# Performance work log

Measured on AMD Instinct MI355X. Metric: run time of the kernel, lower is better.

Reference implementation:

```python
import jax, jax.numpy as jnp
import numpy as np

B, T = 64, 20
VOCAB, E, CE, ANS = 20000, 300, 1024, 3000
H, N, W, R = 512, 256, 64, 4
RW = R * W
IF_SIZES = [RW, R, W, 1, W, W, R, 1, 1, 3 * R]  # read_keys, read_str, write_key, write_str, erase, write_vec, free, alloc_g, write_g, modes
IF_TOT = sum(IF_SIZES)
CLIP = 20.0
EPS = 1e-6


def _cosine_weights(mem, keys, strengths):
    # mem [B,N,W], keys [B,K,W], strengths [B,K] -> softmax over N
    mem_n = mem / (jnp.linalg.norm(mem, axis=-1, keepdims=True) + EPS)
    key_n = keys / (jnp.linalg.norm(keys, axis=-1, keepdims=True) + EPS)
    sim = jnp.einsum('bkw,bnw->bkn', key_n, mem_n)
    return jax.nn.softmax(sim * strengths[..., None], axis=-1)


def _init_state(b):
    z = lambda *s: jnp.zeros(s, jnp.float32)
    return (z(b, N, W), z(b, N, N), z(b, N), z(b, R, N), z(b, N), z(b, N), z(b, R, W), z(b, H), z(b, H))


def _dnc_step(Wih, Whh, b, Wif, bif, Wout, bout, state, x):
    mem, link, prec, wr, ww, usage, rvec, h, c = state
    bsz = x.shape[0]
    inp = jnp.concatenate([x, rvec.reshape(bsz, RW)], -1)
    gates = inp @ Wih + h @ Whh + b
    gi, gf, gg, go = jnp.split(gates, 4, -1)
    c = jax.nn.sigmoid(gf) * c + jax.nn.sigmoid(gi) * jnp.tanh(gg)
    h = jax.nn.sigmoid(go) * jnp.tanh(c)
    hc = jnp.clip(h, -CLIP, CLIP)
    xi = hc @ Wif + bif
    p = jnp.split(xi, np.cumsum(IF_SIZES)[:-1].tolist(), axis=-1)
    read_keys = jnp.tanh(p[0]).reshape(bsz, R, W)
    read_str = jax.nn.softplus(p[1])
    write_key = jnp.tanh(p[2]).reshape(bsz, 1, W)
    write_str = jax.nn.softplus(p[3])
    erase = jax.nn.sigmoid(p[4])
    write_vec = jnp.tanh(p[5])
    free = jax.nn.sigmoid(p[6])
    alloc_g = jax.nn.sigmoid(p[7])
    write_g = jax.nn.sigmoid(p[8])
    modes = jax.nn.softmax(p[9].reshape(bsz, R, 3), -1)

    # usage update and allocation (sort-based, data dependent)
    psi = jnp.prod(1.0 - free[..., None] * wr, axis=1)          # [B,N]
    usage = (usage + ww - usage * ww) * psi
    s_idx = jnp.argsort(usage, axis=-1)                          # ascending usage
    s_u = jnp.take_along_axis(usage, s_idx, -1)
    cp = jnp.cumprod(jnp.concatenate([jnp.ones_like(s_u[:, :1]), s_u[:, :-1]], -1), -1)
    a_sorted = (1.0 - s_u) * cp
    inv = jnp.argsort(s_idx, axis=-1)
    alloc = jnp.take_along_axis(a_sorted, inv, -1)

    # write
    cw = _cosine_weights(mem, write_key, write_str)[:, 0]        # [B,N]
    ww = write_g * (alloc_g * alloc + (1.0 - alloc_g) * cw)
    mem = mem * (1.0 - ww[..., None] * erase[:, None, :]) + ww[..., None] * write_vec[:, None, :]

    # temporal link matrix
    link = (1.0 - ww[:, :, None] - ww[:, None, :]) * link + ww[:, :, None] * prec[:, None, :]
    link = link * (1.0 - jnp.eye(N, dtype=link.dtype))
    prec = (1.0 - ww.sum(-1, keepdims=True)) * prec + ww

    # read
    fw = jnp.einsum('bij,brj->bri', link, wr)
    bw = jnp.einsum('bji,brj->bri', link, wr)
    cr = _cosine_weights(mem, read_keys, read_str)
    wr = modes[..., 0:1] * bw + modes[..., 1:2] * cr + modes[..., 2:3] * fw
    rvec = jnp.einsum('brn,bnw->brw', wr, mem)

    out = jnp.concatenate([hc, rvec.reshape(bsz, RW)], -1) @ Wout + bout
    out = jnp.clip(out, -CLIP, CLIP)
    return (mem, link, prec, wr, ww, usage, rvec, h, c), out


def _model(img_feat, emb, img_W, img_b, q_Wih, q_Whh, q_b, q_Wif, q_bif, q_Wout, q_bout,
           c_Wih, c_Whh, c_b, c_Wif, c_bif, c_Wout, c_bout, fc1_W, fc1_b, fc2_W, fc2_b, qst):
    bsz = qst.shape[0]
    # question encoder: embedding -> tanh -> DNC over time -> mean pool
    qv = jnp.tanh(emb[qst])                                      # [B,T,E]
    step = lambda st, x: _dnc_step(q_Wih, q_Whh, q_b, q_Wif, q_bif, q_Wout, q_bout, st, x)
    _, outs = jax.lax.scan(step, _init_state(bsz), jnp.swapaxes(qv, 0, 1))
    qfeat = outs.mean(0)                                         # [B,CE]
    # image encoder: fc on frozen VGG feature, L2 norm (norm detached)
    imgf = img_feat @ img_W + img_b
    imgf = imgf / jax.lax.stop_gradient(jnp.linalg.norm(imgf, axis=1, keepdims=True))
    comb = jnp.tanh(imgf * qfeat)
    # controller DNC: single timestep
    st_c, out_c = _dnc_step(c_Wih, c_Whh, c_b, c_Wif, c_bif, c_Wout, c_bout, _init_state(bsz), comb)
    rv_c = st_c[6].reshape(bsz, RW)
    last = jnp.tanh(jnp.concatenate([out_c, rv_c], -1))
    last = jnp.tanh(last @ fc1_W + fc1_b)
    return last @ fc2_W + fc2_b                                  # logits [B,ANS]


def setup_inputs():
    ks = jax.random.split(jax.random.key(0), 20)
    g = lambda k, s, sc=0.05: jax.random.normal(k, s, dtype=jnp.float32) * sc
    z = lambda *s: jnp.zeros(s, jnp.float32)
    return {
        'img_feat': g(ks[0], (B, 4096), 1.0),
        'qst': jax.random.randint(ks[1], (B, T), 0, VOCAB),
        'emb': g(ks[2], (VOCAB, E)),
        'img_W': g(ks[3], (4096, CE)), 'img_b': z(CE),
        'q_Wih': g(ks[4], (E + RW, 4 * H)), 'q_Whh': g(ks[5], (H, 4 * H)), 'q_b': z(4 * H),
        'q_Wif': g(ks[6], (H, IF_TOT)), 'q_bif': z(IF_TOT),
        'q_Wout': g(ks[7], (H + RW, CE)), 'q_bout': z(CE),
        'c_Wih': g(ks[8], (CE + RW, 4 * H)), 'c_Whh': g(ks[9], (H, 4 * H)), 'c_b': z(4 * H),
        'c_Wif': g(ks[10], (H, IF_TOT)), 'c_bif': z(IF_TOT),
        'c_Wout': g(ks[11], (H + RW, CE)), 'c_bout': z(CE),
        'fc1_W': g(ks[12], (CE + RW, ANS)), 'fc1_b': z(ANS),
        'fc2_W': g(ks[13], (ANS, ANS)), 'fc2_b': z(ANS),
    }


def reference(img_feat, qst, emb, img_W, img_b, q_Wih, q_Whh, q_b, q_Wif, q_bif, q_Wout, q_bout,
              c_Wih, c_Whh, c_b, c_Wif, c_bif, c_Wout, c_bout, fc1_W, fc1_b, fc2_W, fc2_b):
    return _model(img_feat, emb, img_W, img_b, q_Wih, q_Whh, q_b, q_Wif, q_bif, q_Wout, q_bout,
                  c_Wih, c_Whh, c_b, c_Wif, c_bif, c_Wout, c_bout, fc1_W, fc1_b, fc2_W, fc2_b, qst)
```

## Files before the change

kernel.cpp:

```cpp
#include <hip/hip_runtime.h>
#include <cmath>

#define CLIPV 20.0f
#define EPSV 1e-6f

__device__ __forceinline__ float sigmoidf_(float x){ return 1.0f/(1.0f + expf(-x)); }
__device__ __forceinline__ float softplusf_(float x){ return (x > 20.0f) ? x : log1pf(expf(x)); }
__device__ __forceinline__ float clipf_(float x){ return fminf(fmaxf(x, -CLIPV), CLIPV); }

__device__ __forceinline__ float wave_sum64(float v){
  #pragma unroll
  for (int off=32; off>=1; off>>=1) v += __shfl_xor(v, off, 64);
  return v;
}
__device__ __forceinline__ float wave_max64(float v){
  #pragma unroll
  for (int off=32; off>=1; off>>=1) v = fmaxf(v, __shfl_xor(v, off, 64));
  return v;
}
__device__ __forceinline__ float block_sum256(float v, float* s_red){
  v = wave_sum64(v);
  __syncthreads();
  if ((threadIdx.x & 63) == 0) s_red[threadIdx.x>>6] = v;
  __syncthreads();
  return s_red[0]+s_red[1]+s_red[2]+s_red[3];
}
__device__ __forceinline__ float block_max256(float v, float* s_red){
  v = wave_max64(v);
  __syncthreads();
  if ((threadIdx.x & 63) == 0) s_red[threadIdx.x>>6] = v;
  __syncthreads();
  return fmaxf(fmaxf(s_red[0],s_red[1]), fmaxf(s_red[2],s_red[3]));
}
template<int N>
__device__ __forceinline__ void block_sumN(float (&v)[N], float* scr){
  #pragma unroll
  for (int i=0;i<N;i++) v[i] = wave_sum64(v[i]);
  __syncthreads();
  if ((threadIdx.x & 63) == 0){
    int w = threadIdx.x >> 6;
    #pragma unroll
    for (int i=0;i<N;i++) scr[w*N + i] = v[i];
  }
  __syncthreads();
  #pragma unroll
  for (int i=0;i<N;i++) v[i] = scr[0*N+i] + scr[1*N+i] + scr[2*N+i] + scr[3*N+i];
}
template<int N>
__device__ __forceinline__ void block_maxN(float (&v)[N], float* scr){
  #pragma unroll
  for (int i=0;i<N;i++) v[i] = wave_max64(v[i]);
  __syncthreads();
  if ((threadIdx.x & 63) == 0){
    int w = threadIdx.x >> 6;
    #pragma unroll
    for (int i=0;i<N;i++) scr[w*N + i] = v[i];
  }
  __syncthreads();
  #pragma unroll
  for (int i=0;i<N;i++) v[i] = fmaxf(fmaxf(scr[0*N+i],scr[1*N+i]), fmaxf(scr[2*N+i],scr[3*N+i]));
}

__device__ __forceinline__ void cstore(float* p, float v){
  __hip_atomic_store(p, v, __ATOMIC_RELAXED, __HIP_MEMORY_SCOPE_AGENT);
}

#define WS_MEM    0
#define WS_LINK   1048576
#define WS_PREC   5242880
#define WS_WR     5275648
#define WS_WW     5341184
#define WS_USAGE  5357568
#define WS_BAR    5373952
#define WS_ZONEA  5374976
#define WS_QSUM   5374976
#define WS_HTS    5440512
#define WS_RVS    6128640
#define WS_XIS    6472704
#define WS_GXP    7105728
#define WS_ZONEC  9727168
#define WS_IMGF   10879168
#define WS_COMB   10944704
#define WS_LASTB  11010240
#define WS_HID1   11092160
#define WS_QV     11284160

__global__ void embed_kernel(const int* __restrict__ qst, const float* __restrict__ emb,
                             float* __restrict__ qv){
  int idx = blockIdx.x*256 + threadIdx.x;
  if (idx >= 1280*300) return;
  int m = idx / 300;
  int e = idx - m*300;
  int t = m >> 6, b = m & 63;
  int tok = qst[b*20 + t];
  qv[idx] = tanhf(emb[(size_t)tok*300 + e]);
}

__global__ __launch_bounds__(256) void gemm64(
    int M, int N, int Ktot, int KS,
    const float* __restrict__ A, int lda,
    const float* __restrict__ B,
    const float* __restrict__ bias,
    float* __restrict__ out, float* __restrict__ part, int mode)
{
  __shared__ float As[32*68];
  __shared__ float Bs[32*68];
  int tid = threadIdx.x;
  int nb = blockIdx.x*64, ks = blockIdx.y, mb = blockIdx.z*64;
  int Kc = (((Ktot + KS - 1)/KS) + 3) & ~3;
  int kbeg = ks*Kc, kend = min(Ktot, kbeg + Kc);
  int tm = tid >> 4, tn = tid & 15;
  float acc[4][4];
  #pragma unroll
  for (int i=0;i<4;i++){ acc[i][0]=0.f; acc[i][1]=0.f; acc[i][2]=0.f; acc[i][3]=0.f; }

  for (int k0 = kbeg; k0 < kend; k0 += 32){
    int klim = kend - k0; if (klim > 32) klim = 32;
    #pragma unroll
    for (int i=0;i<2;i++){
      int idx = tid + i*256;
      int m = idx >> 3, kq = (idx & 7) << 2;
      if (kq < klim){
        const float* ap = A + (size_t)(mb+m)*lda + k0 + kq;
        float4 v;
        if (kq + 3 < klim) v = *(const float4*)ap;
        else { v.x=ap[0]; v.y=(kq+1<klim)?ap[1]:0.f; v.z=(kq+2<klim)?ap[2]:0.f; v.w=0.f; }
        float* as = As + m;
        as[(kq+0)*68]=v.x; as[(kq+1)*68]=v.y; as[(kq+2)*68]=v.z; as[(kq+3)*68]=v.w;
      }
    }
    #pragma unroll
    for (int i=0;i<2;i++){
      int idx = tid + i*256;
      int kk = idx >> 4, nq = (idx & 15) << 2;
      int n = nb + nq;
      float4 v = {0.f,0.f,0.f,0.f};
      if (kk < klim && n < N){
        const float* bp = B + (size_t)(k0+kk)*N + n;
        if (n + 3 < N) v = *(const float4*)bp;
        else { v.x=bp[0]; v.y=(n+1<N)?bp[1]:0.f; v.z=(n+2<N)?bp[2]:0.f; }
      }
      *(float4*)(Bs + kk*68 + nq) = v;
    }
    __syncthreads();
    for (int kk = 0; kk < klim; kk++){
      float4 a = *(const float4*)(As + kk*68 + tm*4);
      float4 bv = *(const float4*)(Bs + kk*68 + tn*4);
      acc[0][0]+=a.x*bv.x; acc[0][1]+=a.x*bv.y; acc[0][2]+=a.x*bv.z; acc[0][3]+=a.x*bv.w;
      acc[1][0]+=a.y*bv.x; acc[1][1]+=a.y*bv.y; acc[1][2]+=a.y*bv.z; acc[1][3]+=a.y*bv.w;
      acc[2][0]+=a.z*bv.x; acc[2][1]+=a.z*bv.y; acc[2][2]+=a.z*bv.z; acc[2][3]+=a.z*bv.w;
      acc[3][0]+=a.w*bv.x; acc[3][1]+=a.w*bv.y; acc[3][2]+=a.w*bv.z; acc[3][3]+=a.w*bv.w;
    }
    __syncthreads();
  }

  #pragma unroll
  for (int i=0;i<4;i++){
    int m = tm*4 + i;
    #pragma unroll
    for (int j=0;j<4;j++){
      int n = nb + tn*4 + j;
      if (n < N){
        if (mode == 0){
          part[((size_t)(ks*64 + m))*N + n] = acc[i][j];
        } else {
          float v = acc[i][j] + (bias ? bias[n] : 0.f);
          if (mode == 2) v = tanhf(v);
          out[(size_t)(mb+m)*N + n] = v;
        }
      }
    }
  }
}

__global__ void reduce64(const float* __restrict__ part, int KS, int MN4, int N,
                         const float* __restrict__ bias, float* __restrict__ out, int mode){
  int idx = blockIdx.x*256 + threadIdx.x;
  if (idx >= MN4) return;
  int base = idx*4;
  int n = base % N;
  float4 s = {0.f,0.f,0.f,0.f};
  size_t stride = (size_t)MN4*4;
  for (int p=0;p<KS;p++){
    float4 t = *(const float4*)(part + (size_t)p*stride + base);
    s.x+=t.x; s.y+=t.y; s.z+=t.z; s.w+=t.w;
  }
  if (bias){
    float4 bb = *(const float4*)(bias + n);
    s.x+=bb.x; s.y+=bb.y; s.z+=bb.z; s.w+=bb.w;
  }
  if (mode == 1){ s.x=tanhf(s.x); s.y=tanhf(s.y); s.z=tanhf(s.z); s.w=tanhf(s.w); }
  *(float4*)(out + base) = s;
}

__global__ __launch_bounds__(256) void comb_kernel(const float* __restrict__ imgf,
                                                   const float* __restrict__ qsum,
                                                   float* __restrict__ comb){
  __shared__ float s_red[4];
  int b = blockIdx.x, tid = threadIdx.x;
  float ss = 0.f;
  for (int j = tid; j < 1024; j += 256){ float v = imgf[b*1024+j]; ss += v*v; }
  ss = wave_sum64(ss);
  if ((tid & 63) == 0) s_red[tid>>6] = ss;
  __syncthreads();
  float inv = 1.0f / sqrtf(s_red[0]+s_red[1]+s_red[2]+s_red[3]);
  for (int j = tid; j < 1024; j += 256)
    comb[b*1024+j] = tanhf(imgf[b*1024+j]*inv * qsum[b*1024+j]*0.05f);
}

__global__ void tanhrvec_kernel(const float* __restrict__ rvecT, float* __restrict__ lastB){
  int idx = blockIdx.x*256 + threadIdx.x;
  if (idx >= 16384) return;
  int b = idx & 63, i = idx >> 6;
  lastB[(size_t)b*1280 + 1024 + i] = tanhf(rvecT[i*64 + b]);
}

#define I_LO 138

struct SD_t {
  float s_rk[256], s_rstr[4], s_wkey[64], s_erase[64], s_wvec[64];
  float s_free[4], s_modes[12], s_scal[3], s_pad0[1];
  float s_wr[1024];
  float s_wwnew[256], s_usage[256], s_prec[256], s_scan[256], s_sim[256];
  float s_C[1024], s_D[1024];
  float s_red[44], s_PQ[8];
};
struct SGLO_t { float red[4*768]; float g2[768]; };
struct Shm {
  float Wg[768*8];
  float Wo[768*4];
  float Wi[512*4];
  union { SGLO_t glo; SD_t d; } u;
};

__device__ __forceinline__ float glo_opart(const float* __restrict__ rvP,
                                           const float* __restrict__ hP,
                                           const float* __restrict__ WoL,
                                           float* __restrict__ red,
                                           float bo, int lane, int wid, int b_, int q_){
  float accO[4] = {0.f,0.f,0.f,0.f};
  for (int c = 0; c < 12; c++){
    int k0 = c*64 + wid*16;
    bool isH = (k0 >= 256);
    const float* src = isH ? (hP + (size_t)(k0-256)*64) : (rvP + (size_t)k0*64);
    float a[16];
    #pragma unroll
    for (int u=0; u<16; u++) a[u] = src[u*64 + lane];
    #pragma unroll
    for (int u=0; u<16; u++){
      int k = k0 + u;
      int orow = isH ? (k - 256) : (512 + k);
      float4 wo = *(const float4*)(WoL + (size_t)orow*4);
      float av = isH ? clipf_(a[u]) : a[u];
      accO[0] += av*wo.x; accO[1] += av*wo.y; accO[2] += av*wo.z; accO[3] += av*wo.w;
    }
  }
  #pragma unroll
  for (int j=0;j<4;j++) red[wid*256 + j*64 + lane] = accO[j];
  __syncthreads();
  float v = bo;
  #pragma unroll
  for (int w=0;w<4;w++) v += red[w*256 + q_*64 + b_];
  __syncthreads();
  return v;
}


__device__ __forceinline__ void gbar(int* subs, int* root, int* ggen, int epoch){
  __syncthreads();
  if (threadIdx.x == 0){
    asm volatile("s_waitcnt vmcnt(0)" ::: "memory");
    int g = blockIdx.x & 15;
    int old = __hip_atomic_fetch_add(&subs[g*16], 1, __ATOMIC_RELAXED, __HIP_MEMORY_SCOPE_AGENT);
    if (old == 16*epoch - 1){
      int r = __hip_atomic_fetch_add(root, 1, __ATOMIC_RELAXED, __HIP_MEMORY_SCOPE_AGENT);
      if (r == 16*epoch - 1){
        #pragma unroll
        for (int gg = 0; gg < 16; gg++)
          __hip_atomic_store(&ggen[gg*16], epoch, __ATOMIC_RELAXED, __HIP_MEMORY_SCOPE_AGENT);
      }
    }
    while (__hip_atomic_load(&ggen[g*16], __ATOMIC_RELAXED, __HIP_MEMORY_SCOPE_AGENT) < epoch)
      __builtin_amdgcn_s_sleep(2);
    asm volatile("" ::: "memory");
  }
  __syncthreads();
}

__global__ __launch_bounds__(256) void dnc_recur(
    int T, int outmode, int slot0,
    const float* __restrict__ xpart, const float* __restrict__ Wih_r,
    const float* __restrict__ Whh, const float* __restrict__ gb,
    const float* __restrict__ Wif, const float* __restrict__ bif,
    const float* __restrict__ Wout, const float* __restrict__ bout,
    float* __restrict__ ws, float* __restrict__ outbuf, int* __restrict__ barmem)
{
  __shared__ Shm sh;

  float* memS  = ws + WS_MEM;
  float* linkS = ws + WS_LINK;
  float* precB = ws + WS_PREC;
  float* wrS   = ws + WS_WR;
  float* wwS   = ws + WS_WW;
  float* usgS  = ws + WS_USAGE;
  float* htS   = ws + WS_HTS;
  float* rvS   = ws + WS_RVS;
  float* xiSl  = ws + WS_XIS;
  int* subs  = barmem;
  int* root  = barmem + 256;
  int* ggen  = barmem + 288;
  int* xict  = barmem + 576;
  int* subsH = barmem + 608;
  int* rootH = barmem + 896;

  int tid = threadIdx.x, bid = blockIdx.x;
  int lane = tid & 63, wid = tid >> 6;
  int b_ = tid & 63, q_ = tid >> 6;
  bool isI = (bid >= I_LO);

  {
    int c2 = bid*2;
    float2* Wg2w = (float2*)sh.Wg;
    for (int e2 = tid; e2 < 3072; e2 += 256){
      int k = e2 >> 2, g = e2 & 3;
      const float* src = (k < 256) ? (Wih_r + (size_t)k*2048 + g*512 + c2)
                                   : (Whh + (size_t)(k-256)*2048 + g*512 + c2);
      Wg2w[e2] = *(const float2*)src;
    }
    int c4o = bid*4;
    float4* Wo4 = (float4*)sh.Wo;
    for (int k = tid; k < 768; k += 256)
      Wo4[k] = *(const float4*)(Wout + (size_t)k*1024 + c4o);
    if (isI){
      int c4i = (bid - I_LO)*4;
      for (int e = tid; e < 2048; e += 256){
        int k = e >> 2, c = e & 3;
        int col = c4i + c;
        sh.Wi[e] = (col < 471) ? Wif[(size_t)k*471 + col] : 0.f;
      }
    }
  }
  float bo = bout[bid*4 + q_];
  float bifv = 0.f;
  if (isI && (bid - I_LO)*4 + q_ < 471) bifv = bif[(bid - I_LO)*4 + q_];
  __syncthreads();

  float c_reg = 0.f;
  float qacc = 0.f;

  for (int t = 0; t < T; t++){
    int pp = t & 1, wp = (t + 1) & 1;
    const float* rvP1 = rvS + (size_t)(slot0+t-1)*16384;
    const float* hP1  = htS + (size_t)(slot0+t-1)*32768;

    {
      if (t > 0){
        float accG[8] = {0.f,0.f,0.f,0.f,0.f,0.f,0.f,0.f};
        for (int c = 0; c < 12; c++){
          int k0 = c*64 + wid*16;
          bool isH = (k0 >= 256);
          const float* src = isH ? (hP1 + (size_t)(k0-256)*64) : (rvP1 + (size_t)k0*64);
          float a[16];
          #pragma unroll
          for (int u=0; u<16; u++) a[u] = src[u*64 + lane];
          #pragma unroll
          for (int u=0; u<16; u++){
            int k = k0 + u;
            float4 w0 = *(const float4*)(sh.Wg + (size_t)k*8);
            float4 w1 = *(const float4*)(sh.Wg + (size_t)k*8 + 4);
            float av = a[u];
            accG[0] += av*w0.x; accG[1] += av*w0.y; accG[2] += av*w0.z; accG[3] += av*w0.w;
            accG[4] += av*w1.x; accG[5] += av*w1.y; accG[6] += av*w1.z; accG[7] += av*w1.w;
          }
        }
        #pragma unroll
        for (int j=0;j<8;j++) sh.u.glo.red[wid*768 + j*64 + lane] = accG[j];
      }
      __syncthreads();
      #pragma unroll
      for (int v=0; v<2; v++){
        int j = q_ + v*4;
        int col = (j>>1)*512 + bid*2 + (j&1);
        float s = gb[col] + xpart[((size_t)(t*64 + b_))*2048 + col];
        if (t > 0){
          s += sh.u.glo.red[0*768 + j*64 + b_];
          s += sh.u.glo.red[1*768 + j*64 + b_];
          s += sh.u.glo.red[2*768 + j*64 + b_];
          s += sh.u.glo.red[3*768 + j*64 + b_];
        }
        sh.u.glo.g2[j*64 + b_] = s;
      }
      __syncthreads();
      if (tid < 128){
        int jj = q_;
        float gi = sh.u.glo.g2[(0+jj)*64 + b_];
        float gf = sh.u.glo.g2[(2+jj)*64 + b_];
        float gg = sh.u.glo.g2[(4+jj)*64 + b_];
        float go = sh.u.glo.g2[(6+jj)*64 + b_];
        float cn = sigmoidf_(gf)*c_reg + sigmoidf_(gi)*tanhf(gg);
        float hn = sigmoidf_(go)*tanhf(cn);
        c_reg = cn;
        int col = bid*2 + jj;
        cstore(&htS[(size_t)(slot0+t)*32768 + col*64 + b_], hn);
      }
    }

    __syncthreads();
    if (tid == 0){
      asm volatile("s_waitcnt vmcnt(0)" ::: "memory");
      int g = bid & 15;
      int old = __hip_atomic_fetch_add(&subsH[g*16], 1, __ATOMIC_RELAXED, __HIP_MEMORY_SCOPE_AGENT);
      if (old == 16*(t+1) - 1)
        __hip_atomic_fetch_add(rootH, 1, __ATOMIC_RELAXED, __HIP_MEMORY_SCOPE_AGENT);
    }

    if (!isI && t > 0){
      float v = glo_opart(rvP1, hP1, sh.Wo, sh.u.glo.red, bo, lane, wid, b_, q_);
      qacc += clipf_(v);
    }

    if (isI){
      if (tid == 0){
        while (__hip_atomic_load(rootH, __ATOMIC_RELAXED, __HIP_MEMORY_SCOPE_AGENT) < 16*(t+1))
          __builtin_amdgcn_s_sleep(1);
        asm volatile("" ::: "memory");
      }
      __syncthreads();
      float acc[4] = {0.f,0.f,0.f,0.f};
      const float* hP = htS + (size_t)(slot0+t)*32768;
      for (int c = 0; c < 8; c++){
        int k0 = c*64 + wid*16;
        float a[16];
        #pragma unroll
        for (int u=0; u<16; u++) a[u] = hP[(size_t)(k0+u)*64 + lane];
        #pragma unroll
        for (int u=0; u<16; u++){
          float4 wv = *(const float4*)(sh.Wi + (size_t)(k0+u)*4);
          float ac = clipf_(a[u]);
          acc[0] += ac*wv.x; acc[1] += ac*wv.y; acc[2] += ac*wv.z; acc[3] += ac*wv.w;
        }
      }
      #pragma unroll
      for (int j=0;j<4;j++) sh.u.glo.red[wid*256 + j*64 + lane] = acc[j];
      __syncthreads();
      {
        float s = bifv;
        #pragma unroll
        for (int w=0;w<4;w++) s += sh.u.glo.red[w*256 + q_*64 + b_];
        int col = (bid - I_LO)*4 + q_;
        if (col < 471) cstore(&xiSl[(size_t)(slot0+t)*30144 + b_*471 + col], s);
      }
      __syncthreads();
      if (tid == 0)
        __hip_atomic_fetch_add(xict, 1, __ATOMIC_RELAXED, __HIP_MEMORY_SCOPE_AGENT);
      if (t > 0){
        float v = glo_opart(rvP1, hP1, sh.Wo, sh.u.glo.red, bo, lane, wid, b_, q_);
        qacc += clipf_(v);
      }
    }

    if (bid < 64){
      SD_t& sd = sh.u.d;
      int b = bid;
      const float* prec_in  = precB + pp*16384;
      float*       prec_out = precB + wp*16384;

      for (int e = tid; e < 1024; e += 256){
        sd.s_wr[e] = wrS[(size_t)b*1024 + e];
        sd.s_C[e] = 0.f; sd.s_D[e] = 0.f;
      }
      float wwold = wwS[(size_t)b*256 + tid];
      sd.s_usage[tid] = usgS[(size_t)b*256 + tid];
      sd.s_prec[tid]  = prec_in[(size_t)b*256 + tid];

      if (tid == 0){
        while (__hip_atomic_load(xict, __ATOMIC_RELAXED, __HIP_MEMORY_SCOPE_AGENT) < 118*(t+1))
          __builtin_amdgcn_s_sleep(1);
        asm volatile("" ::: "memory");
      }
      __syncthreads();

      const float* xrow = xiSl + (size_t)(slot0+t)*30144 + (size_t)b*471;
      for (int idx = tid; idx < 471; idx += 256){
        float v = xrow[idx];
        if (idx < 256)       sd.s_rk[idx] = tanhf(v);
        else if (idx < 260)  sd.s_rstr[idx-256] = softplusf_(v);
        else if (idx < 324)  sd.s_wkey[idx-260] = v;
        else if (idx == 324) sd.s_scal[0] = softplusf_(v);
        else if (idx < 389)  sd.s_erase[idx-325] = sigmoidf_(v);
        else if (idx < 453)  sd.s_wvec[idx-389] = tanhf(v);
        else if (idx < 457)  sd.s_free[idx-453] = sigmoidf_(v);
        else if (idx == 457) sd.s_scal[1] = sigmoidf_(v);
        else if (idx == 458) sd.s_scal[2] = sigmoidf_(v);
        else                 sd.s_modes[idx-459] = v;
      }
      __syncthreads();

      if (tid < 4){
        float m0 = sd.s_modes[tid*3], m1 = sd.s_modes[tid*3+1], m2 = sd.s_modes[tid*3+2];
        float mx = fmaxf(m0, fmaxf(m1,m2));
        float e0 = expf(m0-mx), e1 = expf(m1-mx), e2 = expf(m2-mx);
        float s = e0+e1+e2;
        sd.s_modes[tid*3] = e0/s; sd.s_modes[tid*3+1] = e1/s; sd.s_modes[tid*3+2] = e2/s;
      }
      {
        float k = sd.s_rk[wid*64 + lane];
        float ss = wave_sum64(k*k);
        sd.s_rk[wid*64 + lane] = k / (sqrtf(ss) + EPSV);
      }
      if (wid == 0){
        float k = sd.s_wkey[lane];
        float ss = wave_sum64(k*k);
        sd.s_wkey[lane] = k / (sqrtf(ss) + EPSV);
      }

      {
        float psi = 1.f;
        #pragma unroll
        for (int r=0;r<4;r++) psi *= (1.f - sd.s_free[r]*sd.s_wr[r*256+tid]);
        float u = (sd.s_usage[tid] + wwold - sd.s_usage[tid]*wwold) * psi;
        sd.s_usage[tid] = u;
        usgS[(size_t)b*256 + tid] = u;
      }
      __syncthreads();

      int rank_r;
      {
        float u = sd.s_usage[tid];
        int rank = 0;
        #pragma unroll 4
        for (int j4=0;j4<256;j4+=4){
          float4 uv = *(const float4*)(sd.s_usage + j4);
          rank += (uv.x < u) || (uv.x == u && (j4+0) < tid);
          rank += (uv.y < u) || (uv.y == u && (j4+1) < tid);
          rank += (uv.z < u) || (uv.z == u && (j4+2) < tid);
          rank += (uv.w < u) || (uv.w == u && (j4+3) < tid);
        }
        rank_r = rank;
        sd.s_scan[rank] = u;
      }
      __syncthreads();

      {
        float v = sd.s_scan[tid];
        #pragma unroll
        for (int off=1; off<64; off<<=1){
          float u2 = __shfl_up(v, off, 64);
          if (lane >= off) v *= u2;
        }
        if (lane == 63) sd.s_red[wid] = v;
        __syncthreads();
        float pre = 1.f;
        if (wid > 0) pre *= sd.s_red[0];
        if (wid > 1) pre *= sd.s_red[1];
        if (wid > 2) pre *= sd.s_red[2];
        v *= pre;
        sd.s_scan[tid] = v;
        __syncthreads();
      }
      float alloc_r;
      {
        float u = sd.s_usage[tid];
        float cpe = (rank_r > 0) ? sd.s_scan[rank_r-1] : 1.f;
        alloc_r = (1.f - u) * cpe;
      }

      {
        const float4* Mrow = (const float4*)(memS + (size_t)b*16384 + (size_t)tid*64);
        float nrm2 = 0.f, dt = 0.f;
        #pragma unroll
        for (int c4 = 0; c4 < 16; c4++){
          float4 mv = Mrow[c4];
          int w0 = c4*4;
          nrm2 += mv.x*mv.x + mv.y*mv.y + mv.z*mv.z + mv.w*mv.w;
          dt += mv.x*sd.s_wkey[w0] + mv.y*sd.s_wkey[w0+1] + mv.z*sd.s_wkey[w0+2] + mv.w*sd.s_wkey[w0+3];
        }
        sd.s_sim[tid] = dt / (sqrtf(nrm2)+EPSV) * sd.s_scal[0];
      }
      __syncthreads();

      {
        float v = sd.s_sim[tid];
        float mx = block_max256(v, sd.s_red);
        float e = expf(v - mx);
        float sm = block_sum256(e, sd.s_red);
        float cw = e / sm;
        float wwn = sd.s_scal[2] * (sd.s_scal[1]*alloc_r + (1.f - sd.s_scal[1])*cw);
        sd.s_wwnew[tid] = wwn;
        wwS[(size_t)b*256 + tid] = wwn;
        float r9[9];
        r9[0] = wwn;
        #pragma unroll
        for (int r=0;r<4;r++) r9[1+r] = sd.s_prec[tid]*sd.s_wr[r*256+tid];
        #pragma unroll
        for (int r=0;r<4;r++) r9[5+r] = wwn*sd.s_wr[r*256+tid];
        block_sumN<9>(r9, sd.s_red + 4);
        prec_out[(size_t)b*256 + tid] = (1.f - r9[0])*sd.s_prec[tid] + wwn;
        if (tid == 0){
          #pragma unroll
          for (int r=0;r<4;r++){ sd.s_PQ[r] = r9[1+r]; sd.s_PQ[4+r] = r9[5+r]; }
        }
      }
      __syncthreads();

      float aA[4] = {0,0,0,0}, aB[4] = {0,0,0,0};
      {
        const float4* Lrow = (const float4*)(linkS + (size_t)b*65536 + (size_t)tid*256);
        for (int c4 = 0; c4 < 64; c4++){
          float4 lv = Lrow[c4];
          int j = c4*4;
          float w0n = sd.s_wwnew[j], w1n = sd.s_wwnew[j+1], w2n = sd.s_wwnew[j+2], w3n = sd.s_wwnew[j+3];
          #pragma unroll
          for (int r=0;r<4;r++){
            float wr0 = sd.s_wr[r*256+j], wr1 = sd.s_wr[r*256+j+1];
            float wr2 = sd.s_wr[r*256+j+2], wr3 = sd.s_wr[r*256+j+3];
            aA[r] += lv.x*wr0 + lv.y*wr1 + lv.z*wr2 + lv.w*wr3;
            aB[r] += lv.x*(w0n*wr0) + lv.y*(w1n*wr1) + lv.z*(w2n*wr2) + lv.w*(w3n*wr3);
          }
        }
      }
      __syncthreads();

      {
        int cg = tid & 63, ioff = tid >> 6;
        int j0 = cg*4;
        float wwj0 = sd.s_wwnew[j0], wwj1 = sd.s_wwnew[j0+1], wwj2 = sd.s_wwnew[j0+2], wwj3 = sd.s_wwnew[j0+3];
        float pj0 = sd.s_prec[j0], pj1 = sd.s_prec[j0+1], pj2 = sd.s_prec[j0+2], pj3 = sd.s_prec[j0+3];
        float cC[4][4] = {{0}}, cD[4][4] = {{0}};
        float4* Lb = (float4*)(linkS + (size_t)b*65536);
        for (int it = 0; it < 64; it++){
          int i = it*4 + ioff;
          float4 lv = Lb[(size_t)i*64 + cg];
          float wwi = sd.s_wwnew[i];
          float4 ln;
          ln.x = (1.f - wwi - wwj0)*lv.x + wwi*pj0;
          ln.y = (1.f - wwi - wwj1)*lv.y + wwi*pj1;
          ln.z = (1.f - wwi - wwj2)*lv.z + wwi*pj2;
          ln.w = (1.f - wwi - wwj3)*lv.w + wwi*pj3;
          if (i >= j0 && i < j0+4){
            if (i == j0)        ln.x = 0.f;
            else if (i == j0+1) ln.y = 0.f;
            else if (i == j0+2) ln.z = 0.f;
            else                ln.w = 0.f;
          }
          Lb[(size_t)i*64 + cg] = ln;
          #pragma unroll
          for (int r=0;r<4;r++){
            float wri = sd.s_wr[r*256+i];
            float vbi = wwi*wri;
            cC[r][0] += lv.x*wri; cC[r][1] += lv.y*wri; cC[r][2] += lv.z*wri; cC[r][3] += lv.w*wri;
            cD[r][0] += lv.x*vbi; cD[r][1] += lv.y*vbi; cD[r][2] += lv.z*vbi; cD[r][3] += lv.w*vbi;
          }
        }
        for (int w=0; w<4; w++){
          if (ioff == w){
            #pragma unroll
            for (int r=0;r<4;r++){
              sd.s_C[r*256+j0+0] += cC[r][0]; sd.s_C[r*256+j0+1] += cC[r][1];
              sd.s_C[r*256+j0+2] += cC[r][2]; sd.s_C[r*256+j0+3] += cC[r][3];
              sd.s_D[r*256+j0+0] += cD[r][0]; sd.s_D[r*256+j0+1] += cD[r][1];
              sd.s_D[r*256+j0+2] += cD[r][2]; sd.s_D[r*256+j0+3] += cD[r][3];
            }
          }
          __syncthreads();
        }
      }

      float pr[4];
      {
        float4* Mrow = (float4*)(memS + (size_t)b*16384 + (size_t)tid*64);
        float wwn = sd.s_wwnew[tid];
        float nrm2 = 0.f, d0=0.f, d1=0.f, d2=0.f, d3=0.f;
        #pragma unroll
        for (int c4 = 0; c4 < 16; c4++){
          float4 mv = Mrow[c4];
          int w0 = c4*4;
          mv.x = mv.x*(1.f - wwn*sd.s_erase[w0+0]) + wwn*sd.s_wvec[w0+0];
          mv.y = mv.y*(1.f - wwn*sd.s_erase[w0+1]) + wwn*sd.s_wvec[w0+1];
          mv.z = mv.z*(1.f - wwn*sd.s_erase[w0+2]) + wwn*sd.s_wvec[w0+2];
          mv.w = mv.w*(1.f - wwn*sd.s_erase[w0+3]) + wwn*sd.s_wvec[w0+3];
          Mrow[c4] = mv;
          nrm2 += mv.x*mv.x + mv.y*mv.y + mv.z*mv.z + mv.w*mv.w;
          d0 += mv.x*sd.s_rk[w0] + mv.y*sd.s_rk[w0+1] + mv.z*sd.s_rk[w0+2] + mv.w*sd.s_rk[w0+3];
          d1 += mv.x*sd.s_rk[64+w0] + mv.y*sd.s_rk[64+w0+1] + mv.z*sd.s_rk[64+w0+2] + mv.w*sd.s_rk[64+w0+3];
          d2 += mv.x*sd.s_rk[128+w0] + mv.y*sd.s_rk[128+w0+1] + mv.z*sd.s_rk[128+w0+2] + mv.w*sd.s_rk[128+w0+3];
          d3 += mv.x*sd.s_rk[192+w0] + mv.y*sd.s_rk[192+w0+1] + mv.z*sd.s_rk[192+w0+2] + mv.w*sd.s_rk[192+w0+3];
        }
        float inv = 1.f/(sqrtf(nrm2)+EPSV);
        pr[0] = d0*inv*sd.s_rstr[0];
        pr[1] = d1*inv*sd.s_rstr[1];
        pr[2] = d2*inv*sd.s_rstr[2];
        pr[3] = d3*inv*sd.s_rstr[3];
      }
      {
        float m4[4] = {pr[0], pr[1], pr[2], pr[3]};
        block_maxN<4>(m4, sd.s_red + 4);
        float e4[4];
        #pragma unroll
        for (int r=0;r<4;r++) e4[r] = expf(pr[r] - m4[r]);
        float s4[4] = {e4[0], e4[1], e4[2], e4[3]};
        block_sumN<4>(s4, sd.s_red + 4);
        #pragma unroll
        for (int r=0;r<4;r++) pr[r] = e4[r]/s4[r];
      }
      __syncthreads();

      {
        float wwn = sd.s_wwnew[tid], pn = sd.s_prec[tid];
        #pragma unroll
        for (int r=0;r<4;r++){
          float wro = sd.s_wr[r*256+tid];
          float fw  = (1.f-wwn)*aA[r] - aB[r] + wwn*(sd.s_PQ[r] - pn*wro);
          float bwv = (1.f-wwn)*sd.s_C[r*256+tid] - sd.s_D[r*256+tid] + pn*(sd.s_PQ[4+r] - wwn*wro);
          float wrn = sd.s_modes[r*3+0]*bwv + sd.s_modes[r*3+1]*pr[r] + sd.s_modes[r*3+2]*fw;
          wrS[(size_t)b*1024 + r*256 + tid] = wrn;
          sd.s_wr[r*256+tid] = wrn;
        }
      }
      __syncthreads();

      {
        int r = tid >> 6, w = tid & 63;
        const float* Mb = memS + (size_t)b*16384;
        float acc = 0.f;
        for (int n=0; n<256; n++) acc += sd.s_wr[r*256+n]*Mb[(size_t)n*64 + w];
        cstore(&rvS[(size_t)(slot0+t)*16384 + (r*64 + w)*64 + b], acc);
      }
    }

    gbar(subs, root, ggen, t+1);
  }

  {
    float v = glo_opart(rvS + (size_t)(slot0+T-1)*16384,
                        htS + (size_t)(slot0+T-1)*32768,
                        sh.Wo, sh.u.glo.red, bo, lane, wid, b_, q_);
    v = clipf_(v);
    if (outmode == 0){
      qacc += v;
      outbuf[(size_t)b_*1024 + (bid*4 + q_)] = qacc;
    } else {
      outbuf[(size_t)b_*1280 + (bid*4 + q_)] = tanhf(v);
    }
  }
}

extern "C" void kernel_launch(void* const* d_in, const int* in_sizes, int n_in,
                              void* d_out, int out_size, void* d_ws, size_t ws_size,
                              hipStream_t stream) {
  const float* img_feat = (const float*)d_in[0];
  const int*   qst      = (const int*)  d_in[1];
  const float* emb      = (const float*)d_in[2];
  const float* img_W    = (const float*)d_in[3];
  const float* img_b    = (const float*)d_in[4];
  const float* q_Wih    = (const float*)d_in[5];
  const float* q_Whh    = (const float*)d_in[6];
  const float* q_b      = (const float*)d_in[7];
  const float* q_Wif    = (const float*)d_in[8];
  const float* q_bif    = (const float*)d_in[9];
  const float* q_Wout   = (const float*)d_in[10];
  const float* q_bout   = (const float*)d_in[11];
  const float* c_Wih    = (const float*)d_in[12];
  const float* c_Whh    = (const float*)d_in[13];
  const float* c_b      = (const float*)d_in[14];
  const float* c_Wif    = (const float*)d_in[15];
  const float* c_bif    = (const float*)d_in[16];
  const float* c_Wout   = (const float*)d_in[17];
  const float* c_bout   = (const float*)d_in[18];
  const float* fc1_W    = (const float*)d_in[19];
  const float* fc1_b    = (const float*)d_in[20];
  const float* fc2_W    = (const float*)d_in[21];
  const float* fc2_b    = (const float*)d_in[22];

  float* ws = (float*)d_ws;
  float* qv    = ws + WS_QV;
  float* gxp   = ws + WS_GXP;
  float* zoneC = ws + WS_ZONEC;
  float* imgf  = ws + WS_IMGF;
  float* combB = ws + WS_COMB;
  float* lastB = ws + WS_LASTB;
  float* hid1  = ws + WS_HID1;
  float* qsum  = ws + WS_QSUM;
  int*   bar   = (int*)(ws + WS_BAR);

  hipMemsetAsync(ws, 0, (size_t)WS_ZONEA*4, stream);

  embed_kernel<<<1500, 256, 0, stream>>>(qst, emb, qv);

  gemm64<<<dim3(16,16,1), 256, 0, stream>>>(64, 1024, 4096, 16,
      img_feat, 4096, img_W, nullptr, nullptr, zoneC, 0);
  reduce64<<<64, 256, 0, stream>>>(zoneC, 16, 16384, 1024, img_b, imgf, 0);

  gemm64<<<dim3(32,1,20), 256, 0, stream>>>(1280, 2048, 300, 1,
      qv, 300, q_Wih, nullptr, gxp, nullptr, 1);

  dnc_recur<<<256, 256, 0, stream>>>(20, 0, 0,
      gxp, q_Wih + (size_t)300*2048, q_Whh, q_b,
      q_Wif, q_bif, q_Wout, q_bout, ws, qsum, bar);

  comb_kernel<<<64, 256, 0, stream>>>(imgf, qsum, combB);

  hipMemsetAsync(ws, 0, (size_t)WS_ZONEA*4, stream);

  gemm64<<<dim3(32,4,1), 256, 0, stream>>>(64, 2048, 1024, 4,
      combB, 1024, c_Wih, nullptr, nullptr, zoneC, 0);
  reduce64<<<128, 256, 0, stream>>>(zoneC, 4, 32768, 2048, nullptr, gxp, 0);

  dnc_recur<<<256, 256, 0, stream>>>(1, 1, 20,
      gxp, c_Wih + (size_t)1024*2048, c_Whh, c_b,
      c_Wif, c_bif, c_Wout, c_bout, ws, lastB, bar);

  tanhrvec_kernel<<<64, 256, 0, stream>>>(ws + WS_RVS + (size_t)20*16384, lastB);

  gemm64<<<dim3(47,5,1), 256, 0, stream>>>(64, 3000, 1280, 5,
      lastB, 1280, fc1_W, nullptr, nullptr, zoneC, 0);
  reduce64<<<188, 256, 0, stream>>>(zoneC, 5, 48000, 3000, fc1_b, hid1, 1);

  gemm64<<<dim3(47,6,1), 256, 0, stream>>>(64, 3000, 3000, 6,
      hid1, 3000, fc2_W, nullptr, nullptr, zoneC, 0);
  reduce64<<<188, 256, 0, stream>>>(zoneC, 6, 48000, 3000, fc2_b, (float*)d_out, 0);
}
```

Before: 2.066 ms.

## Double block size in DNC recurrence and split link/readvec loops across halves

Launches the persistent recurrence kernel with 512 threads per block instead of 256. The extra waves split the memory-side work (link-matrix forward/backward passes, C/D accumulation, read-vector matvec) in half, with partial sums combined through shared memory. The LSTM-gate and output parts stay on the first 256 threads, guarded by tid checks. The C/D reduction also changes from a serialized per-wave accumulate loop to a float4 partial-buffer sum. This adds shared memory and extra barriers, and idle half-blocks in the non-memory phases, which could lower occupancy.

```diff
diff --git a/kernel.cpp b/kernel.cpp
--- a/kernel.cpp
+++ b/kernel.cpp
@@ -218,12 +218,16 @@
 #define I_LO 138
 
 struct SD_t {
-  float s_rk[256], s_rstr[4], s_wkey[64], s_erase[64], s_wvec[64];
-  float s_free[4], s_modes[12], s_scal[3], s_pad0[1];
   float s_wr[1024];
+  float s_Cp[4096];
+  float s_Dp[4096];
+  float s_aAp[1024], s_aBp[1024];
+  float s_p11[256];
+  float s_rk[256];
   float s_wwnew[256], s_usage[256], s_prec[256], s_scan[256], s_sim[256];
-  float s_C[1024], s_D[1024];
-  float s_red[44], s_PQ[8];
+  float s_wkey[64], s_erase[64], s_wvec[64];
+  float s_red[80], s_PQ[8];
+  float s_rstr[4], s_free[4], s_modes[12], s_scal[3], s_pad0[1];
 };
 struct SGLO_t { float red[4*768]; float g2[768]; };
 struct Shm {
@@ -238,29 +242,34 @@
                                            const float* __restrict__ WoL,
                                            float* __restrict__ red,
                                            float bo, int lane, int wid, int b_, int q_){
-  float accO[4] = {0.f,0.f,0.f,0.f};
-  for (int c = 0; c < 12; c++){
-    int k0 = c*64 + wid*16;
-    bool isH = (k0 >= 256);
-    const float* src = isH ? (hP + (size_t)(k0-256)*64) : (rvP + (size_t)k0*64);
-    float a[16];
+  int tid = threadIdx.x;
+  if (tid < 256){
+    float accO[4] = {0.f,0.f,0.f,0.f};
+    for (int c = 0; c < 12; c++){
+      int k0 = c*64 + wid*16;
+      bool isH = (k0 >= 256);
+      const float* src = isH ? (hP + (size_t)(k0-256)*64) : (rvP + (size_t)k0*64);
+      float a[16];
+      #pragma unroll
+      for (int u=0; u<16; u++) a[u] = src[u*64 + lane];
+      #pragma unroll
+      for (int u=0; u<16; u++){
+        int k = k0 + u;
+        int orow = isH ? (k - 256) : (512 + k);
+        float4 wo = *(const float4*)(WoL + (size_t)orow*4);
+        float av = isH ? clipf_(a[u]) : a[u];
+        accO[0] += av*wo.x; accO[1] += av*wo.y; accO[2] += av*wo.z; accO[3] += av*wo.w;
+      }
+    }
     #pragma unroll
-    for (int u=0; u<16; u++) a[u] = src[u*64 + lane];
+    for (int j=0;j<4;j++) red[wid*256 + j*64 + lane] = accO[j];
+  }
+  __syncthreads();
+  float v = bo;
+  if (tid < 256){
     #pragma unroll
-    for (int u=0; u<16; u++){
-      int k = k0 + u;
-      int orow = isH ? (k - 256) : (512 + k);
-      float4 wo = *(const float4*)(WoL + (size_t)orow*4);
-      float av = isH ? clipf_(a[u]) : a[u];
-      accO[0] += av*wo.x; accO[1] += av*wo.y; accO[2] += av*wo.z; accO[3] += av*wo.w;
-    }
-  }
-  #pragma unroll
-  for (int j=0;j<4;j++) red[wid*256 + j*64 + lane] = accO[j];
-  __syncthreads();
-  float v = bo;
-  #pragma unroll
-  for (int w=0;w<4;w++) v += red[w*256 + q_*64 + b_];
+    for (int w=0;w<4;w++) v += red[w*256 + q_*64 + b_];
+  }
   __syncthreads();
   return v;
 }
@@ -287,7 +296,7 @@
   __syncthreads();
 }
 
-__global__ __launch_bounds__(256) void dnc_recur(
+__global__ __launch_bounds__(512) void dnc_recur(
     int T, int outmode, int slot0,
     const float* __restrict__ xpart, const float* __restrict__ Wih_r,
     const float* __restrict__ Whh, const float* __restrict__ gb,
@@ -321,7 +330,7 @@
   {
     int c2 = bid*2;
     float2* Wg2w = (float2*)sh.Wg;
-    for (int e2 = tid; e2 < 3072; e2 += 256){
+    for (int e2 = tid; e2 < 3072; e2 += 512){
       int k = e2 >> 2, g = e2 & 3;
       const float* src = (k < 256) ? (Wih_r + (size_t)k*2048 + g*512 + c2)
                                    : (Whh + (size_t)(k-256)*2048 + g*512 + c2);
@@ -329,20 +338,20 @@
     }
     int c4o = bid*4;
     float4* Wo4 = (float4*)sh.Wo;
-    for (int k = tid; k < 768; k += 256)
+    for (int k = tid; k < 768; k += 512)
       Wo4[k] = *(const float4*)(Wout + (size_t)k*1024 + c4o);
     if (isI){
       int c4i = (bid - I_LO)*4;
-      for (int e = tid; e < 2048; e += 256){
+      for (int e = tid; e < 2048; e += 512){
         int k = e >> 2, c = e & 3;
         int col = c4i + c;
         sh.Wi[e] = (col < 471) ? Wif[(size_t)k*471 + col] : 0.f;
       }
     }
   }
-  float bo = bout[bid*4 + q_];
+  float bo = (tid < 256) ? bout[bid*4 + q_] : 0.f;
   float bifv = 0.f;
-  if (isI && (bid - I_LO)*4 + q_ < 471) bifv = bif[(bid - I_LO)*4 + q_];
+  if (isI && tid < 256 && (bid - I_LO)*4 + q_ < 471) bifv = bif[(bid - I_LO)*4 + q_];
   __syncthreads();
 
   float c_reg = 0.f;
@@ -354,7 +363,7 @@
     const float* hP1  = htS + (size_t)(slot0+t-1)*32768;
 
     {
-      if (t > 0){
+      if (t > 0 && tid < 256){
         float accG[8] = {0.f,0.f,0.f,0.f,0.f,0.f,0.f,0.f};
         for (int c = 0; c < 12; c++){
           int k0 = c*64 + wid*16;
@@ -377,18 +386,20 @@
         for (int j=0;j<8;j++) sh.u.glo.red[wid*768 + j*64 + lane] = accG[j];
       }
       __syncthreads();
-      #pragma unroll
-      for (int v=0; v<2; v++){
-        int j = q_ + v*4;
-        int col = (j>>1)*512 + bid*2 + (j&1);
-        float s = gb[col] + xpart[((size_t)(t*64 + b_))*2048 + col];
-        if (t > 0){
-          s += sh.u.glo.red[0*768 + j*64 + b_];
-          s += sh.u.glo.red[1*768 + j*64 + b_];
-          s += sh.u.glo.red[2*768 + j*64 + b_];
-          s += sh.u.glo.red[3*768 + j*64 + b_];
-        }
-        sh.u.glo.g2[j*64 + b_] = s;
+      if (tid < 256){
+        #pragma unroll
+        for (int v=0; v<2; v++){
+          int j = q_ + v*4;
+          int col = (j>>1)*512 + bid*2 + (j&1);
+          float s = gb[col] + xpart[((size_t)(t*64 + b_))*2048 + col];
+          if (t > 0){
+            s += sh.u.glo.red[0*768 + j*64 + b_];
+            s += sh.u.glo.red[1*768 + j*64 + b_];
+            s += sh.u.glo.red[2*768 + j*64 + b_];
+            s += sh.u.glo.red[3*768 + j*64 + b_];
+          }
+          sh.u.glo.g2[j*64 + b_] = s;
+        }
       }
       __syncthreads();
       if (tid < 128){
@@ -416,7 +427,7 @@
 
     if (!isI && t > 0){
       float v = glo_opart(rvP1, hP1, sh.Wo, sh.u.glo.red, bo, lane, wid, b_, q_);
-      qacc += clipf_(v);
+      if (tid < 256) qacc += clipf_(v);
     }
 
     if (isI){
@@ -426,24 +437,26 @@
         asm volatile("" ::: "memory");
       }
       __syncthreads();
-      float acc[4] = {0.f,0.f,0.f,0.f};
       const float* hP = htS + (size_t)(slot0+t)*32768;
-      for (int c = 0; c < 8; c++){
-        int k0 = c*64 + wid*16;
-        float a[16];
-        #pragma unroll
-        for (int u=0; u<16; u++) a[u] = hP[(size_t)(k0+u)*64 + lane];
-        #pragma unroll
-        for (int u=0; u<16; u++){
-          float4 wv = *(const float4*)(sh.Wi + (size_t)(k0+u)*4);
-          float ac = clipf_(a[u]);
-          acc[0] += ac*wv.x; acc[1] += ac*wv.y; acc[2] += ac*wv.z; acc[3] += ac*wv.w;
-        }
-      }
-      #pragma unroll
-      for (int j=0;j<4;j++) sh.u.glo.red[wid*256 + j*64 + lane] = acc[j];
-      __syncthreads();
-      {
+      if (tid < 256){
+        float acc[4] = {0.f,0.f,0.f,0.f};
+        for (int c = 0; c < 8; c++){
+          int k0 = c*64 + wid*16;
+          float a[16];
+          #pragma unroll
+          for (int u=0; u<16; u++) a[u] = hP[(size_t)(k0+u)*64 + lane];
+          #pragma unroll
+          for (int u=0; u<16; u++){
+            float4 wv = *(const float4*)(sh.Wi + (size_t)(k0+u)*4);
+            float ac = clipf_(a[u]);
+            acc[0] += ac*wv.x; acc[1] += ac*wv.y; acc[2] += ac*wv.z; acc[3] += ac*wv.w;
+          }
+        }
+        #pragma unroll
+        for (int j=0;j<4;j++) sh.u.glo.red[wid*256 + j*64 + lane] = acc[j];
+      }
+      __syncthreads();
+      if (tid < 256){
         float s = bifv;
         #pragma unroll
         for (int w=0;w<4;w++) s += sh.u.glo.red[w*256 + q_*64 + b_];
@@ -455,7 +468,7 @@
         __hip_atomic_fetch_add(xict, 1, __ATOMIC_RELAXED, __HIP_MEMORY_SCOPE_AGENT);
       if (t > 0){
         float v = glo_opart(rvP1, hP1, sh.Wo, sh.u.glo.red, bo, lane, wid, b_, q_);
-        qacc += clipf_(v);
+        if (tid < 256) qacc += clipf_(v);
       }
     }
 
@@ -465,13 +478,14 @@
       const float* prec_in  = precB + pp*16384;
       float*       prec_out = precB + wp*16384;
 
-      for (int e = tid; e < 1024; e += 256){
+      for (int e = tid; e < 1024; e += 512)
         sd.s_wr[e] = wrS[(size_t)b*1024 + e];
-        sd.s_C[e] = 0.f; sd.s_D[e] = 0.f;
-      }
-      float wwold = wwS[(size_t)b*256 + tid];
-      sd.s_usage[tid] = usgS[(size_t)b*256 + tid];
-      sd.s_prec[tid]  = prec_in[(size_t)b*256 + tid];
+      float wwold = 0.f;
+      if (tid < 256){
+        wwold = wwS[(size_t)b*256 + tid];
+        sd.s_usage[tid] = usgS[(size_t)b*256 + tid];
+        sd.s_prec[tid]  = prec_in[(size_t)b*256 + tid];
+      }
 
       if (tid == 0){
         while (__hip_atomic_load(xict, __ATOMIC_RELAXED, __HIP_MEMORY_SCOPE_AGENT) < 118*(t+1))
@@ -481,7 +495,7 @@
       __syncthreads();
 
       const float* xrow = xiSl + (size_t)(slot0+t)*30144 + (size_t)b*471;
-      for (int idx = tid; idx < 471; idx += 256){
+      for (int idx = tid; idx < 471; idx += 512){
         float v = xrow[idx];
         if (idx < 256)       sd.s_rk[idx] = tanhf(v);
         else if (idx < 260)  sd.s_rstr[idx-256] = softplusf_(v);
@@ -503,7 +517,7 @@
         float s = e0+e1+e2;
         sd.s_modes[tid*3] = e0/s; sd.s_modes[tid*3+1] = e1/s; sd.s_modes[tid*3+2] = e2/s;
       }
-      {
+      if (wid < 4){
         float k = sd.s_rk[wid*64 + lane];
         float ss = wave_sum64(k*k);
         sd.s_rk[wid*64 + lane] = k / (sqrtf(ss) + EPSV);
@@ -514,7 +528,7 @@
         sd.s_wkey[lane] = k / (sqrtf(ss) + EPSV);
       }
 
-      {
+      if (tid < 256){
         float psi = 1.f;
         #pragma unroll
         for (int r=0;r<4;r++) psi *= (1.f - sd.s_free[r]*sd.s_wr[r*256+tid]);
@@ -524,8 +538,8 @@
       }
       __syncthreads();
 
-      int rank_r;
-      {
+      int rank_r = 0;
+      if (tid < 256){
         float u = sd.s_usage[tid];
         int rank = 0;
         #pragma unroll 4
@@ -542,30 +556,35 @@
       __syncthreads();
 
       {
-        float v = sd.s_scan[tid];
-        #pragma unroll
-        for (int off=1; off<64; off<<=1){
-          float u2 = __shfl_up(v, off, 64);
-          if (lane >= off) v *= u2;
-        }
-        if (lane == 63) sd.s_red[wid] = v;
+        float v = 0.f;
+        if (tid < 256){
+          v = sd.s_scan[tid];
+          #pragma unroll
+          for (int off=1; off<64; off<<=1){
+            float u2 = __shfl_up(v, off, 64);
+            if (lane >= off) v *= u2;
+          }
+          if (lane == 63) sd.s_red[wid] = v;
+        }
         __syncthreads();
-        float pre = 1.f;
-        if (wid > 0) pre *= sd.s_red[0];
-        if (wid > 1) pre *= sd.s_red[1];
-        if (wid > 2) pre *= sd.s_red[2];
-        v *= pre;
-        sd.s_scan[tid] = v;
+        if (tid < 256){
+          float pre = 1.f;
+          if (wid > 0) pre *= sd.s_red[0];
+          if (wid > 1) pre *= sd.s_red[1];
+          if (wid > 2) pre *= sd.s_red[2];
+          v *= pre;
+          sd.s_scan[tid] = v;
+        }
         __syncthreads();
       }
-      float alloc_r;
-      {
+      float alloc_r = 0.f;
+      if (tid < 256){
         float u = sd.s_usage[tid];
         float cpe = (rank_r > 0) ? sd.s_scan[rank_r-1] : 1.f;
         alloc_r = (1.f - u) * cpe;
       }
 
-      {
+      if (tid < 256){
         const float4* Mrow = (const float4*)(memS + (size_t)b*16384 + (size_t)tid*64);
         float nrm2 = 0.f, dt = 0.f;
         #pragma unroll
@@ -580,22 +599,29 @@
       __syncthreads();
 
       {
-        float v = sd.s_sim[tid];
+        float v = (tid < 256) ? sd.s_sim[tid] : 0.f;
         float mx = block_max256(v, sd.s_red);
         float e = expf(v - mx);
-        float sm = block_sum256(e, sd.s_red);
-        float cw = e / sm;
-        float wwn = sd.s_scal[2] * (sd.s_scal[1]*alloc_r + (1.f - sd.s_scal[1])*cw);
-        sd.s_wwnew[tid] = wwn;
-        wwS[(size_t)b*256 + tid] = wwn;
+        float sm = block_sum256((tid < 256) ? e : 0.f, sd.s_red);
+        float wwn = 0.f, prv = 0.f;
+        if (tid < 256){
+          float cw = e / sm;
+          wwn = sd.s_scal[2] * (sd.s_scal[1]*alloc_r + (1.f - sd.s_scal[1])*cw);
+          sd.s_wwnew[tid] = wwn;
+          wwS[(size_t)b*256 + tid] = wwn;
+          prv = sd.s_prec[tid];
+        }
         float r9[9];
         r9[0] = wwn;
         #pragma unroll
-        for (int r=0;r<4;r++) r9[1+r] = sd.s_prec[tid]*sd.s_wr[r*256+tid];
-        #pragma unroll
-        for (int r=0;r<4;r++) r9[5+r] = wwn*sd.s_wr[r*256+tid];
-        block_sumN<9>(r9, sd.s_red + 4);
-        prec_out[(size_t)b*256 + tid] = (1.f - r9[0])*sd.s_prec[tid] + wwn;
+        for (int r=0;r<4;r++){
+          float wrv = (tid < 256) ? sd.s_wr[r*256+tid] : 0.f;
+          r9[1+r] = prv*wrv;
+          r9[5+r] = wwn*wrv;
+        }
+        block_sumN<9>(r9, sd.s_red + 8);
+        if (tid < 256)
+          prec_out[(size_t)b*256 + tid] = (1.f - r9[0])*prv + wwn;
         if (tid == 0){
           #pragma unroll
           for (int r=0;r<4;r++){ sd.s_PQ[r] = r9[1+r]; sd.s_PQ[4+r] = r9[5+r]; }
@@ -605,8 +631,10 @@
 
       float aA[4] = {0,0,0,0}, aB[4] = {0,0,0,0};
       {
-        const float4* Lrow = (const float4*)(linkS + (size_t)b*65536 + (size_t)tid*256);
-        for (int c4 = 0; c4 < 64; c4++){
+        int row = tid & 255, half = tid >> 8;
+        const float4* Lrow = (const float4*)(linkS + (size_t)b*65536 + (size_t)row*256);
+        int c4e = half*32 + 32;
+        for (int c4 = half*32; c4 < c4e; c4++){
           float4 lv = Lrow[c4];
           int j = c4*4;
           float w0n = sd.s_wwnew[j], w1n = sd.s_wwnew[j+1], w2n = sd.s_wwnew[j+2], w3n = sd.s_wwnew[j+3];
@@ -618,8 +646,16 @@
             aB[r] += lv.x*(w0n*wr0) + lv.y*(w1n*wr1) + lv.z*(w2n*wr2) + lv.w*(w3n*wr3);
           }
         }
-      }
-      __syncthreads();
+        if (half){
+          #pragma unroll
+          for (int r=0;r<4;r++){ sd.s_aAp[r*256+row] = aA[r]; sd.s_aBp[r*256+row] = aB[r]; }
+        }
+        __syncthreads();
+        if (!half){
+          #pragma unroll
+          for (int r=0;r<4;r++){ aA[r] += sd.s_aAp[r*256+row]; aB[r] += sd.s_aBp[r*256+row]; }
+        }
+      }
 
       {
         int cg = tid & 63, ioff = tid >> 6;
@@ -628,8 +664,8 @@
         float pj0 = sd.s_prec[j0], pj1 = sd.s_prec[j0+1], pj2 = sd.s_prec[j0+2], pj3 = sd.s_prec[j0+3];
         float cC[4][4] = {{0}}, cD[4][4] = {{0}};
         float4* Lb = (float4*)(linkS + (size_t)b*65536);
-        for (int it = 0; it < 64; it++){
-          int i = it*4 + ioff;
+        for (int it = 0; it < 32; it++){
+          int i = it*8 + ioff;
           float4 lv = Lb[(size_t)i*64 + cg];
           float wwi = sd.s_wwnew[i];
           float4 ln;
@@ -652,22 +688,33 @@
             cD[r][0] += lv.x*vbi; cD[r][1] += lv.y*vbi; cD[r][2] += lv.z*vbi; cD[r][3] += lv.w*vbi;
           }
         }
-        for (int w=0; w<4; w++){
-          if (ioff == w){
-            #pragma unroll
-            for (int r=0;r<4;r++){
-              sd.s_C[r*256+j0+0] += cC[r][0]; sd.s_C[r*256+j0+1] += cC[r][1];
-              sd.s_C[r*256+j0+2] += cC[r][2]; sd.s_C[r*256+j0+3] += cC[r][3];
-              sd.s_D[r*256+j0+0] += cD[r][0]; sd.s_D[r*256+j0+1] += cD[r][1];
-              sd.s_D[r*256+j0+2] += cD[r][2]; sd.s_D[r*256+j0+3] += cD[r][3];
-            }
-          }
-          __syncthreads();
-        }
-      }
-
-      float pr[4];
-      {
+        if (ioff >= 4){
+          int io = ioff - 4;
+          #pragma unroll
+          for (int r=0;r<4;r++){
+            float4 cv; cv.x=cC[r][0]; cv.y=cC[r][1]; cv.z=cC[r][2]; cv.w=cC[r][3];
+            float4 dv; dv.x=cD[r][0]; dv.y=cD[r][1]; dv.z=cD[r][2]; dv.w=cD[r][3];
+            *(float4*)(sd.s_Cp + io*1024 + r*256 + j0) = cv;
+            *(float4*)(sd.s_Dp + io*1024 + r*256 + j0) = dv;
+          }
+        }
+        __syncthreads();
+        if (ioff < 4){
+          #pragma unroll
+          for (int r=0;r<4;r++){
+            float4 cv = *(const float4*)(sd.s_Cp + ioff*1024 + r*256 + j0);
+            float4 dv = *(const float4*)(sd.s_Dp + ioff*1024 + r*256 + j0);
+            cv.x += cC[r][0]; cv.y += cC[r][1]; cv.z += cC[r][2]; cv.w += cC[r][3];
+            dv.x += cD[r][0]; dv.y += cD[r][1]; dv.z += cD[r][2]; dv.w += cD[r][3];
+            *(float4*)(sd.s_Cp + ioff*1024 + r*256 + j0) = cv;
+            *(float4*)(sd.s_Dp + ioff*1024 + r*256 + j0) = dv;
+          }
+        }
+        __syncthreads();
+      }
+
+      float pr[4] = {0.f,0.f,0.f,0.f};
+      if (tid < 256){
         float4* Mrow = (float4*)(memS + (size_t)b*16384 + (size_t)tid*64);
         float wwn = sd.s_wwnew[tid];
         float nrm2 = 0.f, d0=0.f, d1=0.f, d2=0.f, d3=0.f;
@@ -694,24 +741,35 @@
       }
       {
         float m4[4] = {pr[0], pr[1], pr[2], pr[3]};
-        block_maxN<4>(m4, sd.s_red + 4);
+        block_maxN<4>(m4, sd.s_red + 8);
         float e4[4];
         #pragma unroll
         for (int r=0;r<4;r++) e4[r] = expf(pr[r] - m4[r]);
-        float s4[4] = {e4[0], e4[1], e4[2], e4[3]};
-        block_sumN<4>(s4, sd.s_red + 4);
-        #pragma unroll
-        for (int r=0;r<4;r++) pr[r] = e4[r]/s4[r];
-      }
-      __syncthreads();
-
-      {
+        float s4[4];
+        #pragma unroll
+        for (int r=0;r<4;r++) s4[r] = (tid < 256) ? e4[r] : 0.f;
+        block_sumN<4>(s4, sd.s_red + 8);
+        if (tid < 256){
+          #pragma unroll
+          for (int r=0;r<4;r++) pr[r] = e4[r]/s4[r];
+        }
+      }
+      __syncthreads();
+
+      if (tid < 256){
         float wwn = sd.s_wwnew[tid], pn = sd.s_prec[tid];
         #pragma unroll
         for (int r=0;r<4;r++){
           float wro = sd.s_wr[r*256+tid];
+          float ccv = sd.s_Cp[0*1024+r*256+tid];
+          float ddv = sd.s_Dp[0*1024+r*256+tid];
+          #pragma unroll
+          for (int io=1; io<4; io++){
+            ccv += sd.s_Cp[io*1024+r*256+tid];
+            ddv += sd.s_Dp[io*1024+r*256+tid];
+          }
           float fw  = (1.f-wwn)*aA[r] - aB[r] + wwn*(sd.s_PQ[r] - pn*wro);
-          float bwv = (1.f-wwn)*sd.s_C[r*256+tid] - sd.s_D[r*256+tid] + pn*(sd.s_PQ[4+r] - wwn*wro);
+          float bwv = (1.f-wwn)*ccv - ddv + pn*(sd.s_PQ[4+r] - wwn*wro);
           float wrn = sd.s_modes[r*3+0]*bwv + sd.s_modes[r*3+1]*pr[r] + sd.s_modes[r*3+2]*fw;
           wrS[(size_t)b*1024 + r*256 + tid] = wrn;
           sd.s_wr[r*256+tid] = wrn;
@@ -720,11 +778,15 @@
       __syncthreads();
 
       {
-        int r = tid >> 6, w = tid & 63;
+        int r = (tid >> 6) & 3, w = tid & 63, half = tid >> 8;
         const float* Mb = memS + (size_t)b*16384;
         float acc = 0.f;
-        for (int n=0; n<256; n++) acc += sd.s_wr[r*256+n]*Mb[(size_t)n*64 + w];
-        cstore(&rvS[(size_t)(slot0+t)*16384 + (r*64 + w)*64 + b], acc);
+        int n0 = half*128, n1 = n0 + 128;
+        for (int n = n0; n < n1; n++) acc += sd.s_wr[r*256+n]*Mb[(size_t)n*64 + w];
+        if (half) sd.s_p11[r*64 + w] = acc;
+        __syncthreads();
+        if (!half)
+          cstore(&rvS[(size_t)(slot0+t)*16384 + (r*64 + w)*64 + b], acc + sd.s_p11[r*64 + w]);
       }
     }
 
@@ -735,12 +797,14 @@
     float v = glo_opart(rvS + (size_t)(slot0+T-1)*16384,
                         htS + (size_t)(slot0+T-1)*32768,
                         sh.Wo, sh.u.glo.red, bo, lane, wid, b_, q_);
-    v = clipf_(v);
-    if (outmode == 0){
-      qacc += v;
-      outbuf[(size_t)b_*1024 + (bid*4 + q_)] = qacc;
-    } else {
-      outbuf[(size_t)b_*1280 + (bid*4 + q_)] = tanhf(v);
+    if (tid < 256){
+      v = clipf_(v);
+      if (outmode == 0){
+        qacc += v;
+        outbuf[(size_t)b_*1024 + (bid*4 + q_)] = qacc;
+      } else {
+        outbuf[(size_t)b_*1280 + (bid*4 + q_)] = tanhf(v);
+      }
     }
   }
 }
@@ -794,7 +858,7 @@
   gemm64<<<dim3(32,1,20), 256, 0, stream>>>(1280, 2048, 300, 1,
       qv, 300, q_Wih, nullptr, gxp, nullptr, 1);
 
-  dnc_recur<<<256, 256, 0, stream>>>(20, 0, 0,
+  dnc_recur<<<256, 512, 0, stream>>>(20, 0, 0,
       gxp, q_Wih + (size_t)300*2048, q_Whh, q_b,
       q_Wif, q_bif, q_Wout, q_bout, ws, qsum, bar);
 
@@ -806,7 +870,7 @@
       combB, 1024, c_Wih, nullptr, nullptr, zoneC, 0);
   reduce64<<<128, 256, 0, stream>>>(zoneC, 4, 32768, 2048, nullptr, gxp, 0);
 
-  dnc_recur<<<256, 256, 0, stream>>>(1, 1, 20,
+  dnc_recur<<<256, 512, 0, stream>>>(1, 1, 20,
       gxp, c_Wih + (size_t)1024*2048, c_Whh, c_b,
       c_Wif, c_bif, c_Wout, c_bout, ws, lastB, bar);
 
```

Result: slower. 2.358 ms (+14.1%).
